# Kernel optimization log

Hardware: AMD Instinct MI355X
Metric: run time of the kernel (lower is better)

The kernel has to match this reference:

```python
import jax, jax.numpy as jnp
import numpy as np

T, B, H = 2048, 16, 1024


def setup_inputs() -> dict:
    key = jax.random.key(0)
    k1, k2, k3 = jax.random.split(key, 3)
    inputs = jax.random.normal(k1, (T, B, H), dtype=jnp.float32)
    # torch params initialized uniform_(-0.1, 0.1)
    weight_W = jax.random.uniform(k2, (H, H), dtype=jnp.float32, minval=-0.1, maxval=0.1)
    weight_proj = jax.random.uniform(k3, (H, 1), dtype=jnp.float32, minval=-0.1, maxval=0.1)
    return {"inputs": inputs, "weight_W": weight_W, "weight_proj": weight_proj,
            "attention_width": 3}


def reference(inputs, weight_W, weight_proj, attention_width):
    # inputs: [T, B, H] (time-major). For t < w the input passes through unchanged.
    # For t >= w: attend over the previous w steps (t-w .. t-1, excluding t):
    #   score_j = tanh(h_j @ W) @ proj, a = softmax over window, out = sum_j a_j * h_j
    w = attention_width
    t = inputs.shape[0]
    n = t - w  # number of attended output positions
    # per-position scores, computed once for all timesteps: [T, B]
    scores = jnp.squeeze(jnp.tanh(inputs @ weight_W) @ weight_proj, axis=-1)
    # sliding windows via w shifted views (w is small and static)
    s_win = jnp.stack([scores[j:j + n] for j in range(w)], axis=0)   # [w, n, B]
    v_win = jnp.stack([inputs[j:j + n] for j in range(w)], axis=0)   # [w, n, B, H]
    attn = jax.nn.softmax(s_win, axis=0)                             # softmax over window
    tail = jnp.einsum('wnb,wnbh->nbh', attn, v_win)                  # [n, B, H]
    return jnp.concatenate([inputs[:w], tail], axis=0)               # [T, B, H]
```

## Files before the change

kernel.cpp:

```cpp
#include <hip/hip_runtime.h>
#include <stdint.h>

#define T_DIM 2048
#define B_DIM 16
#define H_DIM 1024
#define M_DIM (T_DIM * B_DIM)
#define TCHUNK 32

typedef __attribute__((ext_vector_type(8))) short bf16x8;
typedef __attribute__((ext_vector_type(4))) float floatx4;

#define BARRIER() asm volatile("s_barrier" ::: "memory")
#define LGKM0()                                            \
  do {                                                     \
    asm volatile("s_waitcnt lgkmcnt(0)" ::: "memory");     \
    __builtin_amdgcn_sched_barrier(0);                     \
  } while (0)

__device__ inline unsigned short f2bf(float f) {
  union { float f; unsigned int u; } c; c.f = f;
  unsigned int u = c.u;
  return (unsigned short)((u + 0x7FFFu + ((u >> 16) & 1u)) >> 16);
}

__device__ inline float bf2f(unsigned short u) {
  union { float f; unsigned int u; } c; c.u = ((unsigned int)u) << 16;
  return c.f;
}

__device__ inline float fast_tanh(float x) {
  float e = __expf(2.0f * x);
  return 1.0f - 2.0f / (e + 1.0f);
}

__device__ __forceinline__ void glds16(const unsigned short* g,
                                       const unsigned short* l) {
  __builtin_amdgcn_global_load_lds(
      (const __attribute__((address_space(1))) void*)g,
      (__attribute__((address_space(3))) void*)l, 16, 0, 0);
}

__global__ void convert_x_kernel(const float* __restrict__ x,
                                 unsigned short* __restrict__ xb) {
  size_t i = ((size_t)blockIdx.x * 256 + threadIdx.x) * 4;
  float4 v = *(const float4*)(x + i);
  ushort4 o;
  o.x = f2bf(v.x); o.y = f2bf(v.y); o.z = f2bf(v.z); o.w = f2bf(v.w);
  *(ushort4*)(xb + i) = o;
}

__global__ void transpose_w_kernel(const float* __restrict__ w,
                                   unsigned short* __restrict__ wt) {
  __shared__ float tile[32][33];
  int tx = threadIdx.x, ty = threadIdx.y;
  int n0 = blockIdx.x * 32, k0 = blockIdx.y * 32;
  for (int i = ty; i < 32; i += 8)
    tile[i][tx] = w[(size_t)(k0 + i) * H_DIM + n0 + tx];
  __syncthreads();
  for (int i = ty; i < 32; i += 8)
    wt[(size_t)(n0 + i) * H_DIM + k0 + tx] = f2bf(tile[tx][i]);
}

__global__ __launch_bounds__(512, 2)
void score_gemm_kernel(const unsigned short* __restrict__ Xb,
                       const unsigned short* __restrict__ Wt,
                       const float* __restrict__ proj,
                       float* __restrict__ scores) {
  __shared__ __align__(16) unsigned short ldsA[32768];
  __shared__ __align__(16) unsigned short ldsB[32768];

  const int tid  = threadIdx.x;
  const int lane = tid & 63;
  const int wave = tid >> 6;
  const int wy   = wave >> 2;
  const int wx   = wave & 3;
  const int quad = lane >> 4, l16 = lane & 15;

  const int idx   = blockIdx.x;
  const int x7    = idx & 7;
  const int split = (idx >> 3) & 3;
  const int g     = idx >> 5;
  const int bm    = g * 8 + x7;
  const int m0    = bm * 256;
  const int n0    = split * 256;

  int gOff0, gOff1, lB0, lB1;
  {
    int ci0 = wave * 64 + lane;
    int r0  = ci0 >> 3;
    gOff0 = r0 * H_DIM + (((ci0 & 7) ^ (r0 & 7)) * 8);
    lB0   = (wave * 64) * 8;
    int ci1 = ci0 + 512;
    int r1  = ci1 >> 3;
    gOff1 = r1 * H_DIM + (((ci1 & 7) ^ (r1 & 7)) * 8);
    lB1   = (wave * 64 + 512) * 8;
  }

  const int cg0 = quad ^ (l16 & 7);
  const int cg1 = (quad + 4) ^ (l16 & 7);

  auto issue_ht = [&](int h) {
    int th = h >> 2, ht = h & 3;
    int base = (th & 1) * 16384 + (ht & 1) * 8192;
    int k0 = th * 64;
    if (ht & 2) {
      const unsigned short* gs =
          Xb + (size_t)(m0 + (ht & 1) * 128) * H_DIM + k0;
      glds16(gs + gOff0, &ldsA[base + lB0]);
      glds16(gs + gOff1, &ldsA[base + lB1]);
    } else {
      const unsigned short* gs =
          Wt + (size_t)(n0 + (ht & 1) * 128) * H_DIM + k0;
      glds16(gs + gOff0, &ldsB[base + lB0]);
      glds16(gs + gOff1, &ldsB[base + lB1]);
    }
  };

  floatx4 acc[8][4];
  #pragma unroll
  for (int m = 0; m < 8; ++m)
    #pragma unroll
    for (int n = 0; n < 4; ++n) acc[m][n] = (floatx4){0.f, 0.f, 0.f, 0.f};

  #pragma unroll
  for (int h = 0; h < 6; ++h) issue_ht(h);
  asm volatile("s_waitcnt vmcnt(4)" ::: "memory");
  BARRIER();

  int cur = 0;
  for (int t = 0; t < 16; ++t) {
    const int aB = cur * 16384 + wy * 8192;
    const int bB = cur * 16384 + (wx >> 1) * 8192;
    const int nL = (wx & 1) * 64;

    bf16x8 af[4][2], bfr[2][2][2];

    #pragma unroll
    for (int rs = 0; rs < 4; ++rs) {
      int r = rs * 16 + l16;
      af[rs][0] = *(const bf16x8*)&ldsA[aB + r * 64 + cg0 * 8];
      af[rs][1] = *(const bf16x8*)&ldsA[aB + r * 64 + cg1 * 8];
    }
    #pragma unroll
    for (int ns = 0; ns < 2; ++ns) {
      int n = nL + ns * 16 + l16;
      bfr[0][ns][0] = *(const bf16x8*)&ldsB[bB + n * 64 + cg0 * 8];
      bfr[0][ns][1] = *(const bf16x8*)&ldsB[bB + n * 64 + cg1 * 8];
    }
    { int h = 4 * t + 6; if (h < 64) issue_ht(h); }
    BARRIER();
    LGKM0();
    __builtin_amdgcn_s_setprio(1);
    #pragma unroll
    for (int k = 0; k < 2; ++k)
      #pragma unroll
      for (int rs = 0; rs < 4; ++rs)
        #pragma unroll
        for (int ns = 0; ns < 2; ++ns)
          acc[rs][ns] = __builtin_amdgcn_mfma_f32_16x16x32_bf16(
              af[rs][k], bfr[0][ns][k], acc[rs][ns], 0, 0, 0);
    __builtin_amdgcn_s_setprio(0);
    BARRIER();

    #pragma unroll
    for (int ns = 0; ns < 2; ++ns) {
      int n = nL + 32 + ns * 16 + l16;
      bfr[1][ns][0] = *(const bf16x8*)&ldsB[bB + n * 64 + cg0 * 8];
      bfr[1][ns][1] = *(const bf16x8*)&ldsB[bB + n * 64 + cg1 * 8];
    }
    { int h = 4 * t + 7; if (h < 64) issue_ht(h); }
    BARRIER();
    LGKM0();
    __builtin_amdgcn_s_setprio(1);
    #pragma unroll
    for (int k = 0; k < 2; ++k)
      #pragma unroll
      for (int rs = 0; rs < 4; ++rs)
        #pragma unroll
        for (int ns = 0; ns < 2; ++ns)
          acc[rs][2 + ns] = __builtin_amdgcn_mfma_f32_16x16x32_bf16(
              af[rs][k], bfr[1][ns][k], acc[rs][2 + ns], 0, 0, 0);
    __builtin_amdgcn_s_setprio(0);
    BARRIER();

    #pragma unroll
    for (int rs = 0; rs < 4; ++rs) {
      int r = 64 + rs * 16 + l16;
      af[rs][0] = *(const bf16x8*)&ldsA[aB + r * 64 + cg0 * 8];
      af[rs][1] = *(const bf16x8*)&ldsA[aB + r * 64 + cg1 * 8];
    }
    { int h = 4 * t + 8; if (h < 64) issue_ht(h); }
    BARRIER();
    LGKM0();
    __builtin_amdgcn_s_setprio(1);
    #pragma unroll
    for (int k = 0; k < 2; ++k)
      #pragma unroll
      for (int rs = 0; rs < 4; ++rs)
        #pragma unroll
        for (int ns = 0; ns < 2; ++ns)
          acc[4 + rs][2 + ns] = __builtin_amdgcn_mfma_f32_16x16x32_bf16(
              af[rs][k], bfr[1][ns][k], acc[4 + rs][2 + ns], 0, 0, 0);
    __builtin_amdgcn_s_setprio(0);
    BARRIER();

    { int h = 4 * t + 9; if (h < 64) issue_ht(h); }
    BARRIER();
    LGKM0();
    __builtin_amdgcn_s_setprio(1);
    #pragma unroll
    for (int k = 0; k < 2; ++k)
      #pragma unroll
      for (int rs = 0; rs < 4; ++rs)
        #pragma unroll
        for (int ns = 0; ns < 2; ++ns)
          acc[4 + rs][ns] = __builtin_amdgcn_mfma_f32_16x16x32_bf16(
              af[rs][k], bfr[0][ns][k], acc[4 + rs][ns], 0, 0, 0);
    __builtin_amdgcn_s_setprio(0);
    if (t < 14) asm volatile("s_waitcnt vmcnt(4)" ::: "memory");
    else        asm volatile("s_waitcnt vmcnt(0)" ::: "memory");
    BARRIER();

    cur ^= 1;
  }

  float pv[2][2];
  #pragma unroll
  for (int nq = 0; nq < 2; ++nq)
    #pragma unroll
    for (int ns = 0; ns < 2; ++ns)
      pv[nq][ns] = proj[n0 + wx * 64 + nq * 32 + ns * 16 + l16];

  #pragma unroll
  for (int m = 0; m < 8; ++m)
    #pragma unroll
    for (int gg = 0; gg < 4; ++gg) {
      float v = 0.f;
      #pragma unroll
      for (int nq = 0; nq < 2; ++nq)
        #pragma unroll
        for (int ns = 0; ns < 2; ++ns)
          v += fast_tanh(acc[m][nq * 2 + ns][gg]) * pv[nq][ns];
      v += __shfl_xor(v, 1);
      v += __shfl_xor(v, 2);
      v += __shfl_xor(v, 4);
      v += __shfl_xor(v, 8);
      if (l16 == 0) {
        int row = m0 + wy * 128 + (m >> 2) * 64 + (m & 3) * 16 + quad * 4 + gg;
        atomicAdd(&scores[row], v);
      }
    }
}

__global__ void out_kernel_bf16(const float* __restrict__ x,
                                const unsigned short* __restrict__ xb,
                                const float* __restrict__ scores,
                                const int* __restrict__ wp,
                                float* __restrict__ out) {
  int w = *wp;
  int t0 = blockIdx.x * TCHUNK;
  int b  = blockIdx.y;
  int h  = threadIdx.x;
  const float4* x4 = (const float4*)x;
  float4* o4 = (float4*)out;
  const ushort4* xb4 = (const ushort4*)xb;

  if (w == 3) {
    float4 z = {0.f, 0.f, 0.f, 0.f};
    float4 a0, a1, a2;
    float  s0, s1, s2;
    #pragma unroll
    for (int j = 0; j < 3; ++j) {
      int tm = t0 - 3 + j;
      float4 a = z; float s = 0.f;
      if (tm >= 0) {
        ushort4 u = xb4[((size_t)tm * B_DIM + b) * 256 + h];
        a.x = bf2f(u.x); a.y = bf2f(u.y); a.z = bf2f(u.z); a.w = bf2f(u.w);
        s = scores[tm * B_DIM + b];
      }
      if (j == 0) { a0 = a; s0 = s; }
      else if (j == 1) { a1 = a; s1 = s; }
      else { a2 = a; s2 = s; }
    }
    for (int i = 0; i < TCHUNK; ++i) {
      int t = t0 + i;
      size_t rbase = ((size_t)t * B_DIM + b) * 256 + h;
      ushort4 u = xb4[rbase];
      float4 v;
      v.x = bf2f(u.x); v.y = bf2f(u.y); v.z = bf2f(u.z); v.w = bf2f(u.w);
      float sv = scores[t * B_DIM + b];
      if (t < 3) {
        o4[rbase] = x4[rbase];
      } else {
        float m = fmaxf(fmaxf(s0, s1), s2);
        float e0 = __expf(s0 - m), e1 = __expf(s1 - m), e2 = __expf(s2 - m);
        float inv = 1.0f / (e0 + e1 + e2);
        e0 *= inv; e1 *= inv; e2 *= inv;
        float4 o;
        o.x = e0 * a0.x + e1 * a1.x + e2 * a2.x;
        o.y = e0 * a0.y + e1 * a1.y + e2 * a2.y;
        o.z = e0 * a0.z + e1 * a1.z + e2 * a2.z;
        o.w = e0 * a0.w + e1 * a1.w + e2 * a2.w;
        o4[rbase] = o;
      }
      a0 = a1; a1 = a2; a2 = v;
      s0 = s1; s1 = s2; s2 = sv;
    }
  } else {
    if (w > 8) w = 8;
    for (int i = 0; i < TCHUNK; ++i) {
      int t = t0 + i;
      size_t rbase = ((size_t)t * B_DIM + b) * 256 + h;
      if (t < w) { o4[rbase] = x4[rbase]; continue; }
      float s[8];
      float mx = -1e30f;
      for (int j = 0; j < w; ++j) {
        s[j] = scores[(t - w + j) * B_DIM + b];
        mx = fmaxf(mx, s[j]);
      }
      float sum = 0.f;
      for (int j = 0; j < w; ++j) { s[j] = __expf(s[j] - mx); sum += s[j]; }
      float inv = 1.0f / sum;
      float4 o = {0.f, 0.f, 0.f, 0.f};
      for (int j = 0; j < w; ++j) {
        float a = s[j] * inv;
        float4 v = x4[((size_t)(t - w + j) * B_DIM + b) * 256 + h];
        o.x += a * v.x; o.y += a * v.y; o.z += a * v.z; o.w += a * v.w;
      }
      o4[rbase] = o;
    }
  }
}

__global__ void out_kernel_f32(const float* __restrict__ x,
                               const float* __restrict__ scores,
                               const int* __restrict__ wp,
                               float* __restrict__ out) {
  int w = *wp;
  int t0 = blockIdx.x * TCHUNK;
  int b  = blockIdx.y;
  int h  = threadIdx.x;
  const float4* x4 = (const float4*)x;
  float4* o4 = (float4*)out;

  if (w == 3) {
    float4 z = {0.f, 0.f, 0.f, 0.f};
    float4 a0, a1, a2;
    float  s0, s1, s2;
    {
      int tm = t0 - 3;
      a0 = (tm >= 0) ? x4[((size_t)tm * B_DIM + b) * 256 + h] : z;
      s0 = (tm >= 0) ? scores[tm * B_DIM + b] : 0.f;
      tm = t0 - 2;
      a1 = (tm >= 0) ? x4[((size_t)tm * B_DIM + b) * 256 + h] : z;
      s1 = (tm >= 0) ? scores[tm * B_DIM + b] : 0.f;
      tm = t0 - 1;
      a2 = (tm >= 0) ? x4[((size_t)tm * B_DIM + b) * 256 + h] : z;
      s2 = (tm >= 0) ? scores[tm * B_DIM + b] : 0.f;
    }
    for (int i = 0; i < TCHUNK; ++i) {
      int t = t0 + i;
      size_t rbase = ((size_t)t * B_DIM + b) * 256 + h;
      float4 v = x4[rbase];
      float  sv = scores[t * B_DIM + b];
      if (t < 3) {
        o4[rbase] = v;
      } else {
        float m = fmaxf(fmaxf(s0, s1), s2);
        float e0 = __expf(s0 - m), e1 = __expf(s1 - m), e2 = __expf(s2 - m);
        float inv = 1.0f / (e0 + e1 + e2);
        e0 *= inv; e1 *= inv; e2 *= inv;
        float4 o;
        o.x = e0 * a0.x + e1 * a1.x + e2 * a2.x;
        o.y = e0 * a0.y + e1 * a1.y + e2 * a2.y;
        o.z = e0 * a0.z + e1 * a1.z + e2 * a2.z;
        o.w = e0 * a0.w + e1 * a1.w + e2 * a2.w;
        o4[rbase] = o;
      }
      a0 = a1; a1 = a2; a2 = v;
      s0 = s1; s1 = s2; s2 = sv;
    }
  } else {
    if (w > 8) w = 8;
    for (int i = 0; i < TCHUNK; ++i) {
      int t = t0 + i;
      size_t rbase = ((size_t)t * B_DIM + b) * 256 + h;
      if (t < w) { o4[rbase] = x4[rbase]; continue; }
      float s[8];
      float mx = -1e30f;
      for (int j = 0; j < w; ++j) {
        s[j] = scores[(t - w + j) * B_DIM + b];
        mx = fmaxf(mx, s[j]);
      }
      float sum = 0.f;
      for (int j = 0; j < w; ++j) { s[j] = __expf(s[j] - mx); sum += s[j]; }
      float inv = 1.0f / sum;
      float4 o = {0.f, 0.f, 0.f, 0.f};
      for (int j = 0; j < w; ++j) {
        float a = s[j] * inv;
        float4 v = x4[((size_t)(t - w + j) * B_DIM + b) * 256 + h];
        o.x += a * v.x; o.y += a * v.y; o.z += a * v.z; o.w += a * v.w;
      }
      o4[rbase] = o;
    }
  }
}

extern "C" void kernel_launch(void* const* d_in, const int* in_sizes, int n_in,
                              void* d_out, int out_size, void* d_ws, size_t ws_size,
                              hipStream_t stream) {
  const float* x    = (const float*)d_in[0];
  const float* w    = (const float*)d_in[1];
  const float* proj = (const float*)d_in[2];
  const int*   wp   = (const int*)d_in[3];
  float* out = (float*)d_out;

  const size_t XB_BYTES = (size_t)64 * 1024 * 1024;
  const size_t WT_BYTES = (size_t)2 * 1024 * 1024;
  const size_t need = XB_BYTES + WT_BYTES + (size_t)M_DIM * sizeof(float);
  const bool use_ws = ws_size >= need;

  unsigned short* Xb;
  unsigned short* Wt;
  float* scores;
  if (use_ws) {
    Xb = (unsigned short*)d_ws;
    Wt = (unsigned short*)((char*)d_ws + XB_BYTES);
    scores = (float*)((char*)d_ws + XB_BYTES + WT_BYTES);
  } else {
    Xb = (unsigned short*)d_out;
    Wt = (unsigned short*)((char*)d_out + XB_BYTES);
    scores = (float*)d_ws;
  }

  hipMemsetAsync(scores, 0, M_DIM * sizeof(float), stream);

  convert_x_kernel<<<M_DIM * H_DIM / 1024, 256, 0, stream>>>(x, Xb);
  transpose_w_kernel<<<dim3(32, 32), dim3(32, 8), 0, stream>>>(w, Wt);
  score_gemm_kernel<<<512, 512, 0, stream>>>(Xb, Wt, proj, scores);
  if (use_ws)
    out_kernel_bf16<<<dim3(T_DIM / TCHUNK, B_DIM), 256, 0, stream>>>(x, Xb, scores, wp, out);
  else
    out_kernel_f32<<<dim3(T_DIM / TCHUNK, B_DIM), 256, 0, stream>>>(x, scores, wp, out);
}
```

Before: 343.7 us.

## Merge GEMM k-loop phases from four to two and split LDS waits by k-half

The inner GEMM tile loop now has two barrier-delimited phases per K step instead of four. All B fragments are loaded up front, along with the A fragments for half the rows, and global prefetches are issued in pairs. LDS reads are ordered by k-half, so the first set of MFMAs can start after a partial lgkmcnt wait while the remaining fragments arrive. This cuts barrier count and exposed LDS latency, at the cost of more live registers for the B fragments and reliance on exact lgkmcnt counts matching issue order.

```diff
diff --git a/kernel.cpp b/kernel.cpp
--- a/kernel.cpp
+++ b/kernel.cpp
@@ -11,10 +11,10 @@
 typedef __attribute__((ext_vector_type(4))) float floatx4;
 
 #define BARRIER() asm volatile("s_barrier" ::: "memory")
-#define LGKM0()                                            \
-  do {                                                     \
-    asm volatile("s_waitcnt lgkmcnt(0)" ::: "memory");     \
-    __builtin_amdgcn_sched_barrier(0);                     \
+#define WAIT_LGKM(N)                                              \
+  do {                                                            \
+    asm volatile("s_waitcnt lgkmcnt(" #N ")" ::: "memory");       \
+    __builtin_amdgcn_sched_barrier(0);                            \
   } while (0)
 
 __device__ inline unsigned short f2bf(float f) {
@@ -135,87 +135,89 @@
 
     bf16x8 af[4][2], bfr[2][2][2];
 
+    { int h = 4 * t + 6; if (h < 64) issue_ht(h); }
+    { int h = 4 * t + 7; if (h < 64) issue_ht(h); }
     #pragma unroll
     for (int rs = 0; rs < 4; ++rs) {
       int r = rs * 16 + l16;
       af[rs][0] = *(const bf16x8*)&ldsA[aB + r * 64 + cg0 * 8];
+    }
+    #pragma unroll
+    for (int nq = 0; nq < 2; ++nq)
+      #pragma unroll
+      for (int ns = 0; ns < 2; ++ns) {
+        int n = nL + nq * 32 + ns * 16 + l16;
+        bfr[nq][ns][0] = *(const bf16x8*)&ldsB[bB + n * 64 + cg0 * 8];
+      }
+    __builtin_amdgcn_sched_barrier(0);
+    #pragma unroll
+    for (int rs = 0; rs < 4; ++rs) {
+      int r = rs * 16 + l16;
       af[rs][1] = *(const bf16x8*)&ldsA[aB + r * 64 + cg1 * 8];
     }
     #pragma unroll
-    for (int ns = 0; ns < 2; ++ns) {
-      int n = nL + ns * 16 + l16;
-      bfr[0][ns][0] = *(const bf16x8*)&ldsB[bB + n * 64 + cg0 * 8];
-      bfr[0][ns][1] = *(const bf16x8*)&ldsB[bB + n * 64 + cg1 * 8];
-    }
-    { int h = 4 * t + 6; if (h < 64) issue_ht(h); }
+    for (int nq = 0; nq < 2; ++nq)
+      #pragma unroll
+      for (int ns = 0; ns < 2; ++ns) {
+        int n = nL + nq * 32 + ns * 16 + l16;
+        bfr[nq][ns][1] = *(const bf16x8*)&ldsB[bB + n * 64 + cg1 * 8];
+      }
     BARRIER();
-    LGKM0();
+    WAIT_LGKM(8);
     __builtin_amdgcn_s_setprio(1);
     #pragma unroll
-    for (int k = 0; k < 2; ++k)
-      #pragma unroll
-      for (int rs = 0; rs < 4; ++rs)
+    for (int rs = 0; rs < 4; ++rs)
+      #pragma unroll
+      for (int nq = 0; nq < 2; ++nq)
         #pragma unroll
         for (int ns = 0; ns < 2; ++ns)
-          acc[rs][ns] = __builtin_amdgcn_mfma_f32_16x16x32_bf16(
-              af[rs][k], bfr[0][ns][k], acc[rs][ns], 0, 0, 0);
+          acc[rs][nq * 2 + ns] = __builtin_amdgcn_mfma_f32_16x16x32_bf16(
+              af[rs][0], bfr[nq][ns][0], acc[rs][nq * 2 + ns], 0, 0, 0);
+    WAIT_LGKM(0);
+    #pragma unroll
+    for (int rs = 0; rs < 4; ++rs)
+      #pragma unroll
+      for (int nq = 0; nq < 2; ++nq)
+        #pragma unroll
+        for (int ns = 0; ns < 2; ++ns)
+          acc[rs][nq * 2 + ns] = __builtin_amdgcn_mfma_f32_16x16x32_bf16(
+              af[rs][1], bfr[nq][ns][1], acc[rs][nq * 2 + ns], 0, 0, 0);
     __builtin_amdgcn_s_setprio(0);
     BARRIER();
 
-    #pragma unroll
-    for (int ns = 0; ns < 2; ++ns) {
-      int n = nL + 32 + ns * 16 + l16;
-      bfr[1][ns][0] = *(const bf16x8*)&ldsB[bB + n * 64 + cg0 * 8];
-      bfr[1][ns][1] = *(const bf16x8*)&ldsB[bB + n * 64 + cg1 * 8];
-    }
-    { int h = 4 * t + 7; if (h < 64) issue_ht(h); }
-    BARRIER();
-    LGKM0();
-    __builtin_amdgcn_s_setprio(1);
-    #pragma unroll
-    for (int k = 0; k < 2; ++k)
-      #pragma unroll
-      for (int rs = 0; rs < 4; ++rs)
-        #pragma unroll
-        for (int ns = 0; ns < 2; ++ns)
-          acc[rs][2 + ns] = __builtin_amdgcn_mfma_f32_16x16x32_bf16(
-              af[rs][k], bfr[1][ns][k], acc[rs][2 + ns], 0, 0, 0);
-    __builtin_amdgcn_s_setprio(0);
-    BARRIER();
-
+    { int h = 4 * t + 8; if (h < 64) issue_ht(h); }
+    { int h = 4 * t + 9; if (h < 64) issue_ht(h); }
     #pragma unroll
     for (int rs = 0; rs < 4; ++rs) {
       int r = 64 + rs * 16 + l16;
       af[rs][0] = *(const bf16x8*)&ldsA[aB + r * 64 + cg0 * 8];
+    }
+    __builtin_amdgcn_sched_barrier(0);
+    #pragma unroll
+    for (int rs = 0; rs < 4; ++rs) {
+      int r = 64 + rs * 16 + l16;
       af[rs][1] = *(const bf16x8*)&ldsA[aB + r * 64 + cg1 * 8];
     }
-    { int h = 4 * t + 8; if (h < 64) issue_ht(h); }
     BARRIER();
-    LGKM0();
+    WAIT_LGKM(4);
     __builtin_amdgcn_s_setprio(1);
     #pragma unroll
-    for (int k = 0; k < 2; ++k)
-      #pragma unroll
-      for (int rs = 0; rs < 4; ++rs)
+    for (int rs = 0; rs < 4; ++rs)
+      #pragma unroll
+      for (int nq = 0; nq < 2; ++nq)
         #pragma unroll
         for (int ns = 0; ns < 2; ++ns)
-          acc[4 + rs][2 + ns] = __builtin_amdgcn_mfma_f32_16x16x32_bf16(
-              af[rs][k], bfr[1][ns][k], acc[4 + rs][2 + ns], 0, 0, 0);
-    __builtin_amdgcn_s_setprio(0);
-    BARRIER();
-
-    { int h = 4 * t + 9; if (h < 64) issue_ht(h); }
-    BARRIER();
-    LGKM0();
-    __builtin_amdgcn_s_setprio(1);
-    #pragma unroll
-    for (int k = 0; k < 2; ++k)
-      #pragma unroll
-      for (int rs = 0; rs < 4; ++rs)
+          acc[4 + rs][nq * 2 + ns] = __builtin_amdgcn_mfma_f32_16x16x32_bf16(
+              af[rs][0], bfr[nq][ns][0], acc[4 + rs][nq * 2 + ns], 0, 0, 0);
+    WAIT_LGKM(0);
+    #pragma unroll
+    for (int rs = 0; rs < 4; ++rs)
+      #pragma unroll
+      for (int nq = 0; nq < 2; ++nq)
         #pragma unroll
         for (int ns = 0; ns < 2; ++ns)
-          acc[4 + rs][ns] = __builtin_amdgcn_mfma_f32_16x16x32_bf16(
-              af[rs][k], bfr[0][ns][k], acc[4 + rs][ns], 0, 0, 0);
+          acc[4 + rs][nq * 2 + ns] = __builtin_amdgcn_mfma_f32_16x16x32_bf16(
+              af[rs][1], bfr[nq][ns][1], acc[4 + rs][nq * 2 + ns], 0, 0, 0);
     __builtin_amdgcn_s_setprio(0);
     if (t < 14) asm volatile("s_waitcnt vmcnt(4)" ::: "memory");
     else        asm volatile("s_waitcnt vmcnt(0)" ::: "memory");
```

Result: no change. 346.0 us (+0.7%).
